# Optimization experiments

Measured on AMD Instinct MI355X. Metric: run time of the kernel, lower is better.

## Reference

```python
import jax, jax.numpy as jnp
import numpy as np

B_, L_, DIN, DM, DS, DR, K = 2, 1024, 1024, 2048, 16, 128, 4


def setup_inputs() -> dict:
    key = jax.random.key(0)
    ks = jax.random.split(key, 10)
    s = lambda k, shape, sc=0.02: (jax.random.normal(k, shape, jnp.float32) * sc)
    A_init = jnp.tile(jnp.arange(1, DS + 1, dtype=jnp.float32)[None, :], (DM, 1))  # (DM, DS)
    return {
        'x_in': jax.random.normal(ks[0], (B_, L_, DIN), jnp.float32),
        'W_in': s(ks[1], (DIN, DM)),
        'W_res': s(ks[2], (DIN, DM)),
        'W_out': s(ks[3], (DM, DIN)),
        'conv_w': s(ks[4], (DM, K), 0.1),   # depthwise conv weight (torch shape (DM,1,K) squeezed)
        'conv_b': jnp.zeros((DM,), jnp.float32),
        'A_log': jnp.log(A_init),
        'D': jnp.ones((DM,), jnp.float32),
        'W_B': s(ks[5], (DM, DS)),
        'W_C': s(ks[6], (DM, DS)),
        'W_dt': s(ks[7], (DM, DR)),
        'dt_w': s(ks[8], (DR, DM)),
        'dt_b': jnp.zeros((DM,), jnp.float32),
    }


def reference(x_in, W_in, W_res, W_out, conv_w, conv_b, A_log, D, W_B, W_C, W_dt, dt_w, dt_b):
    Bb, L, _ = x_in.shape
    x = x_in @ W_in                     # (B, L, DM)
    res = x_in @ W_res                  # (B, L, DM)
    # Causal depthwise conv1d: pad left k-1, truncate to L (matches Conv1d(padding=k-1)[:, :, :L])
    xp = jnp.pad(x, ((0, 0), (K - 1, 0), (0, 0)))
    xc = conv_b
    for i in range(K):
        xc = xc + xp[:, i:i + L, :] * conv_w[:, i]
    xc = jax.nn.silu(xc)                # (B, L, DM)
    # Selective SSM (fused_ssm)
    A = -jnp.exp(A_log)                 # (DM, DS)
    Bp = xc @ W_B                       # (B, L, DS)
    Cp = xc @ W_C                       # (B, L, DS)
    delta = jax.nn.softplus((xc @ W_dt) @ dt_w + dt_b)  # (B, L, DM)
    dA = jnp.exp(delta[..., None] * A)                       # (B, L, DM, DS)
    dBu = delta[..., None] * Bp[:, :, None, :] * xc[..., None]  # (B, L, DM, DS)

    def step(h, inp):
        dA_t, dBu_t, C_t = inp
        h = dA_t * h + dBu_t                         # (B, DM, DS)
        y = jnp.einsum('bdn,bn->bd', h, C_t)         # (B, DM)
        return h, y

    h0 = jnp.zeros((Bb, DM, DS), jnp.float32)
    _, ys = jax.lax.scan(step, h0, (dA.transpose(1, 0, 2, 3), dBu.transpose(1, 0, 2, 3), Cp.transpose(1, 0, 2)))
    y = ys.transpose(1, 0, 2) + D * xc  # (B, L, DM)
    y = y * jax.nn.silu(res)
    return y @ W_out                    # (B, L, DIN)
```

## Files before the change

### kernel.cpp

```cpp
#include <hip/hip_runtime.h>
#include <hip/hip_bf16.h>

constexpr int B_  = 2;
constexpr int L_  = 1024;
constexpr int DIN = 1024;
constexpr int DM  = 2048;
constexpr int DS  = 16;
constexpr int DR  = 128;
constexpr int KC  = 4;
constexpr int M_  = B_ * L_;
constexpr int NP2 = 256;
constexpr int NPC = 160;
constexpr int KSLICES = 8;
constexpr int KSL = DM / KSLICES;

constexpr int NC = 32;
constexpr int CL = L_ / NC;
constexpr int S_ = B_ * DM * DS;

typedef __bf16 bf16x8 __attribute__((ext_vector_type(8)));
typedef float  f32x4  __attribute__((ext_vector_type(4)));

__device__ __forceinline__ void gload_lds16(const void* g, void* l) {
    __builtin_amdgcn_global_load_lds(
        (const __attribute__((address_space(1))) void*)g,
        (__attribute__((address_space(3))) void*)l, 16, 0, 0);
}

__device__ __forceinline__ void transpose_block(const float* __restrict__ in,
                                                __bf16* __restrict__ out,
                                                int R, int C, int bx, int by, int t) {
    __shared__ float tile[32][33];
    int tx = t & 31, ty = t >> 5;
    #pragma unroll
    for (int j = 0; j < 32; j += 8)
        tile[ty + j][tx] = in[(size_t)(by * 32 + ty + j) * C + (bx * 32 + tx)];
    __syncthreads();
    #pragma unroll
    for (int j = 0; j < 32; j += 8)
        out[(size_t)(bx * 32 + ty + j) * R + (by * 32 + tx)] = (__bf16)tile[tx][ty + j];
}

__global__ void prep_all(const float* __restrict__ x_in, const float* __restrict__ W_in,
                         const float* __restrict__ W_res, const float* __restrict__ W_out,
                         const float* __restrict__ dt_w,
                         const float* __restrict__ W_B, const float* __restrict__ W_C,
                         const float* __restrict__ W_dt, const float* __restrict__ conv_w,
                         __bf16* __restrict__ xinB, __bf16* __restrict__ WinT,
                         __bf16* __restrict__ WresT, __bf16* __restrict__ WoutT,
                         __bf16* __restrict__ dtwT, __bf16* __restrict__ projW,
                         float* __restrict__ cwT) {
    int blk = blockIdx.x, t = threadIdx.x;
    if (blk < 8192) {
        int i = blk * 256 + t;
        xinB[i] = (__bf16)x_in[i];
    } else if (blk < 10240) {
        int b = blk - 8192;
        transpose_block(W_in, WinT, DIN, DM, b % 64, b / 64, t);
    } else if (blk < 12288) {
        int b = blk - 10240;
        transpose_block(W_res, WresT, DIN, DM, b % 64, b / 64, t);
    } else if (blk < 14336) {
        int b = blk - 12288;
        transpose_block(W_out, WoutT, DM, DIN, b % 32, b / 32, t);
    } else if (blk < 14592) {
        int b = blk - 14336;
        transpose_block(dt_w, dtwT, DR, DM, b % 64, b / 64, t);
    } else if (blk < 16640) {
        int i = (blk - 14592) * 256 + t;
        int k = i % DM;
        int n = i / DM;
        float v = 0.f;
        if (n < 16)        v = W_B[(size_t)k * DS + n];
        else if (n < 32)   v = W_C[(size_t)k * DS + (n - 16)];
        else if (n < 160)  v = W_dt[(size_t)k * DR + (n - 32)];
        projW[i] = (__bf16)v;
    } else {
        int j = (blk - 16640) * 256 + t;
        int tap = j / DM, d = j % DM;
        cwT[j] = conv_w[d * KC + tap];
    }
}

__global__ void reduce_split(const __bf16* __restrict__ PpartB, float* __restrict__ Bp,
                             float* __restrict__ Cp, __bf16* __restrict__ dtmpB) {
    int i = blockIdx.x * 256 + threadIdx.x;
    int row = i / NPC, c = i % NPC;
    float v = 0.f;
    #pragma unroll
    for (int ks = 0; ks < KSLICES; ks++)
        v += (float)PpartB[(size_t)ks * M_ * NPC + i];
    if (c < 16)       Bp[(size_t)row * DS + c] = v;
    else if (c < 32)  Cp[(size_t)row * DS + (c - 16)] = v;
    else              dtmpB[(size_t)row * DR + (c - 32)] = (__bf16)v;
}

template<int EPI>
__global__ void gemm_tile128(const __bf16* __restrict__ A, const __bf16* __restrict__ BT,
                             float* __restrict__ Cf, __bf16* __restrict__ Cb,
                             const float* __restrict__ bias, int M, int N, int K,
                             int lda, int ldb) {
    __shared__ __bf16 sA[2][2][128 * 32];
    __shared__ __bf16 sB[2][2][128 * 32];
    int t = threadIdx.x;
    int lane = t & 63, w = t >> 6;
    int wm = w >> 2, wn = w & 3;
    int m0 = blockIdx.y * 128, n0 = blockIdx.x * 128;
    int kbase = blockIdx.z * K;
    int q = lane >> 4, rr = lane & 15;

    f32x4 acc[4][2] = {};

    int srow = t >> 2;
    int slot = t & 3;

    const int nt = K >> 6;

    auto stage = [&](int kt, int bufi) {
        int gkb = slot ^ ((srow >> 1) & 3);
        #pragma unroll
        for (int s = 0; s < 2; s++) {
            gload_lds16(A  + (size_t)(m0 + srow) * lda + kbase + kt + s * 32 + gkb * 8,
                        &sA[bufi][s][w * 512]);
            gload_lds16(BT + (size_t)(n0 + srow) * ldb + kbase + kt + s * 32 + gkb * 8,
                        &sB[bufi][s][w * 512]);
        }
    };

    stage(0, 0);
    __syncthreads();

    int cur = 0;
    for (int tix = 0; tix < nt; tix++) {
        if (tix + 1 < nt) stage((tix + 1) << 6, cur ^ 1);

        #pragma unroll
        for (int s = 0; s < 2; s++) {
            bf16x8 af[4], bfr[2];
            #pragma unroll
            for (int i = 0; i < 4; i++) {
                int rowA = wm * 64 + i * 16 + rr;
                af[i] = *(const bf16x8*)(&sA[cur][s][rowA * 32 + ((q ^ ((rowA >> 1) & 3)) * 8)]);
            }
            #pragma unroll
            for (int j = 0; j < 2; j++) {
                int rowB = wn * 32 + j * 16 + rr;
                bfr[j] = *(const bf16x8*)(&sB[cur][s][rowB * 32 + ((q ^ ((rowB >> 1) & 3)) * 8)]);
            }
            #pragma unroll
            for (int i = 0; i < 4; i++)
                #pragma unroll
                for (int j = 0; j < 2; j++)
                    acc[i][j] = __builtin_amdgcn_mfma_f32_16x16x32_bf16(af[i], bfr[j], acc[i][j], 0, 0, 0);
        }

        __syncthreads();
        cur ^= 1;
    }

    #pragma unroll
    for (int i = 0; i < 4; i++) {
        #pragma unroll
        for (int j = 0; j < 2; j++) {
            int col = n0 + wn * 32 + j * 16 + rr;
            #pragma unroll
            for (int jj = 0; jj < 4; jj++) {
                int row = m0 + wm * 64 + i * 16 + q * 4 + jj;
                float v = acc[i][j][jj];
                if (EPI == 1) {
                    float z = v + bias[col];
                    Cb[(size_t)row * N + col] = (__bf16)((z > 20.f) ? z : log1pf(__expf(z)));
                } else if (EPI == 2) {
                    if (col < DM) ((__bf16*)Cf)[(size_t)row * DM + col] = (__bf16)v;
                    else          Cb[(size_t)row * DM + (col - DM)] = (__bf16)v;
                } else {
                    if (col < NPC)
                        Cb[(size_t)blockIdx.z * M * NPC + (size_t)row * NPC + col] = (__bf16)v;
                }
            }
        }
    }
}

__global__ void gemm_out64(const __bf16* __restrict__ A, const __bf16* __restrict__ BT,
                           float* __restrict__ C, int M, int N, int K, int lda, int ldb) {
    __shared__ __bf16 sA[2][2][128 * 32];
    __shared__ __bf16 sB[2][2][64 * 32];
    int t = threadIdx.x;
    int lane = t & 63, w = t >> 6;
    int wm = w >> 1, wn = w & 1;
    int m0 = blockIdx.y * 128, n0 = blockIdx.x * 64;
    int q = lane >> 4, rr = lane & 15;

    f32x4 acc[2][2] = {};
    int srow = t >> 2;
    int slot = t & 3;

    const int nt = K >> 6;

    auto stage = [&](int kt, int bufi) {
        int gkb = slot ^ ((srow >> 1) & 3);
        #pragma unroll
        for (int s = 0; s < 2; s++) {
            gload_lds16(A + (size_t)(m0 + srow) * lda + kt + s * 32 + gkb * 8,
                        &sA[bufi][s][w * 512]);
            if (t < 256)
                gload_lds16(BT + (size_t)(n0 + srow) * ldb + kt + s * 32 + gkb * 8,
                            &sB[bufi][s][w * 512]);
        }
    };

    stage(0, 0);
    __syncthreads();

    int cur = 0;
    for (int tix = 0; tix < nt; tix++) {
        if (tix + 1 < nt) stage((tix + 1) << 6, cur ^ 1);

        #pragma unroll
        for (int s = 0; s < 2; s++) {
            bf16x8 af[2], bfr[2];
            #pragma unroll
            for (int i = 0; i < 2; i++) {
                int rowA = wm * 32 + i * 16 + rr;
                af[i] = *(const bf16x8*)(&sA[cur][s][rowA * 32 + ((q ^ ((rowA >> 1) & 3)) * 8)]);
            }
            #pragma unroll
            for (int j = 0; j < 2; j++) {
                int rowB = wn * 32 + j * 16 + rr;
                bfr[j] = *(const bf16x8*)(&sB[cur][s][rowB * 32 + ((q ^ ((rowB >> 1) & 3)) * 8)]);
            }
            #pragma unroll
            for (int i = 0; i < 2; i++)
                #pragma unroll
                for (int j = 0; j < 2; j++)
                    acc[i][j] = __builtin_amdgcn_mfma_f32_16x16x32_bf16(af[i], bfr[j], acc[i][j], 0, 0, 0);
        }

        __syncthreads();
        cur ^= 1;
    }

    #pragma unroll
    for (int i = 0; i < 2; i++) {
        #pragma unroll
        for (int j = 0; j < 2; j++) {
            int col = n0 + wn * 32 + j * 16 + rr;
            #pragma unroll
            for (int jj = 0; jj < 4; jj++) {
                int row = m0 + wm * 32 + i * 16 + q * 4 + jj;
                C[(size_t)row * N + col] = acc[i][j][jj];
            }
        }
    }
}

__global__ void conv_silu(const __bf16* __restrict__ x, const float* __restrict__ cwT,
                          const float* __restrict__ bias, __bf16* __restrict__ xcB) {
    int row = blockIdx.x;
    int d   = threadIdx.x * 8;
    int l   = row % L_;
    size_t base = (size_t)row * DM + d;

    float acc[8];
    {
        const f32x4* b4 = (const f32x4*)(bias + d);
        f32x4 b0 = b4[0], b1 = b4[1];
        #pragma unroll
        for (int q = 0; q < 4; q++) { acc[q] = b0[q]; acc[4 + q] = b1[q]; }
    }
    #pragma unroll
    for (int i = 0; i < KC; i++) {
        int li = l - (KC - 1) + i;
        if (li >= 0) {
            bf16x8 xv = *(const bf16x8*)(x + base + (size_t)(i - (KC - 1)) * DM);
            const f32x4* w4 = (const f32x4*)(cwT + (size_t)i * DM + d);
            f32x4 w0 = w4[0], w1 = w4[1];
            #pragma unroll
            for (int q = 0; q < 4; q++) {
                acc[q]     = fmaf((float)xv[q],     w0[q], acc[q]);
                acc[4 + q] = fmaf((float)xv[4 + q], w1[q], acc[4 + q]);
            }
        }
    }
    bf16x8 out;
    #pragma unroll
    for (int q = 0; q < 8; q++) {
        float v = acc[q] / (1.f + __expf(-acc[q]));
        out[q] = (__bf16)v;
    }
    *(bf16x8*)(xcB + base) = out;
}

__global__ void scan_phase1(const __bf16* __restrict__ delta, const __bf16* __restrict__ xc,
                            const float* __restrict__ Bp, const float* __restrict__ A_log,
                            __bf16* __restrict__ aprodB, __bf16* __restrict__ cendB) {
    int blk = blockIdx.x;
    int c   = blk % NC;
    int rem = blk / NC;
    int dmt = rem % (DM / 256);
    int b   = rem / (DM / 256);
    int t   = threadIdx.x;
    int dm  = dmt * 256 + t;
    int l0  = c * CL;

    __shared__ float sB[CL * DS];
    sB[t]       = Bp[((size_t)b * L_ + l0) * DS + t];
    sB[t + 256] = Bp[((size_t)b * L_ + l0) * DS + t + 256];
    __syncthreads();

    float Aval[DS];
    {
        const f32x4* Ap = (const f32x4*)(A_log + (size_t)dm * DS);
        #pragma unroll
        for (int r4 = 0; r4 < 4; r4++) {
            f32x4 a = Ap[r4];
            #pragma unroll
            for (int q = 0; q < 4; q++) Aval[r4 * 4 + q] = -__expf(a[q]);
        }
    }

    float h[DS], ap[DS];
    #pragma unroll
    for (int i = 0; i < DS; i++) { h[i] = 0.f; ap[i] = 1.f; }

    size_t base = ((size_t)b * L_ + l0) * DM + dm;
    #pragma unroll 4
    for (int j = 0; j < CL; j++) {
        float dl  = (float)delta[base + (size_t)j * DM];
        float xv  = (float)xc[base + (size_t)j * DM];
        float cmn = dl * xv;
        const f32x4* sB4 = (const f32x4*)(sB + j * DS);
        #pragma unroll
        for (int r4 = 0; r4 < 4; r4++) {
            f32x4 bv = sB4[r4];
            #pragma unroll
            for (int q = 0; q < 4; q++) {
                int i = r4 * 4 + q;
                float dA = __expf(dl * Aval[i]);
                ap[i] *= dA;
                h[i] = fmaf(dA, h[i], cmn * bv[q]);
            }
        }
    }

    size_t s = ((size_t)(b * DM + dm)) * DS;
    #pragma unroll
    for (int r8 = 0; r8 < 2; r8++) {
        bf16x8 va, vh;
        #pragma unroll
        for (int q = 0; q < 8; q++) { va[q] = (__bf16)ap[r8 * 8 + q]; vh[q] = (__bf16)h[r8 * 8 + q]; }
        ((bf16x8*)(aprodB + (size_t)c * S_ + s))[r8] = va;
        ((bf16x8*)(cendB  + (size_t)c * S_ + s))[r8] = vh;
    }
}

__global__ void scan_phase2(const __bf16* __restrict__ aprodB, const __bf16* __restrict__ cendB,
                            __bf16* __restrict__ hinitB) {
    int u = blockIdx.x * 256 + threadIdx.x;
    float h = 0.f;
    #pragma unroll
    for (int c = 0; c < NC; c++) {
        float a  = (float)aprodB[(size_t)c * S_ + u];
        float ce = (float)cendB [(size_t)c * S_ + u];
        hinitB[(size_t)c * S_ + u] = (__bf16)h;
        h = fmaf(a, h, ce);
    }
}

__global__ void scan_phase3(const __bf16* __restrict__ delta, const __bf16* __restrict__ xc,
                            const float* __restrict__ Bp, const float* __restrict__ Cp,
                            const __bf16* __restrict__ res, const float* __restrict__ A_log,
                            const float* __restrict__ Dw, const __bf16* __restrict__ hinitB,
                            __bf16* __restrict__ ybar) {
    int blk = blockIdx.x;
    int c   = blk % NC;
    int rem = blk / NC;
    int dmt = rem % (DM / 256);
    int b   = rem / (DM / 256);
    int t   = threadIdx.x;
    int dm  = dmt * 256 + t;
    int l0  = c * CL;

    __shared__ float sB[CL * DS];
    __shared__ float sC[CL * DS];
    sB[t]       = Bp[((size_t)b * L_ + l0) * DS + t];
    sB[t + 256] = Bp[((size_t)b * L_ + l0) * DS + t + 256];
    sC[t]       = Cp[((size_t)b * L_ + l0) * DS + t];
    sC[t + 256] = Cp[((size_t)b * L_ + l0) * DS + t + 256];
    __syncthreads();

    float Aval[DS];
    {
        const f32x4* Ap = (const f32x4*)(A_log + (size_t)dm * DS);
        #pragma unroll
        for (int r4 = 0; r4 < 4; r4++) {
            f32x4 a = Ap[r4];
            #pragma unroll
            for (int q = 0; q < 4; q++) Aval[r4 * 4 + q] = -__expf(a[q]);
        }
    }
    float Dval = Dw[dm];

    float h[DS];
    {
        size_t s = ((size_t)(b * DM + dm)) * DS;
        #pragma unroll
        for (int r8 = 0; r8 < 2; r8++) {
            bf16x8 v = ((const bf16x8*)(hinitB + (size_t)c * S_ + s))[r8];
            #pragma unroll
            for (int q = 0; q < 8; q++) h[r8 * 8 + q] = (float)v[q];
        }
    }

    size_t base = ((size_t)b * L_ + l0) * DM + dm;
    #pragma unroll 4
    for (int j = 0; j < CL; j++) {
        float dl  = (float)delta[base + (size_t)j * DM];
        float xv  = (float)xc[base + (size_t)j * DM];
        float rv  = (float)res[base + (size_t)j * DM];
        float cmn = dl * xv;
        float y = 0.f;
        const f32x4* sB4 = (const f32x4*)(sB + j * DS);
        const f32x4* sC4 = (const f32x4*)(sC + j * DS);
        #pragma unroll
        for (int r4 = 0; r4 < 4; r4++) {
            f32x4 bv = sB4[r4];
            f32x4 cv = sC4[r4];
            #pragma unroll
            for (int q = 0; q < 4; q++) {
                int i = r4 * 4 + q;
                float dA = __expf(dl * Aval[i]);
                h[i] = fmaf(dA, h[i], cmn * bv[q]);
                y = fmaf(h[i], cv[q], y);
            }
        }
        float g = rv / (1.f + __expf(-rv));
        ybar[base + (size_t)j * DM] = (__bf16)((y + Dval * xv) * g);
    }
}

extern "C" void kernel_launch(void* const* d_in, const int* in_sizes, int n_in,
                              void* d_out, int out_size, void* d_ws, size_t ws_size,
                              hipStream_t stream) {
    const float* x_in   = (const float*)d_in[0];
    const float* W_in   = (const float*)d_in[1];
    const float* W_res  = (const float*)d_in[2];
    const float* W_out  = (const float*)d_in[3];
    const float* conv_w = (const float*)d_in[4];
    const float* conv_b = (const float*)d_in[5];
    const float* A_log  = (const float*)d_in[6];
    const float* Dw     = (const float*)d_in[7];
    const float* W_B    = (const float*)d_in[8];
    const float* W_C    = (const float*)d_in[9];
    const float* W_dt   = (const float*)d_in[10];
    const float* dt_w   = (const float*)d_in[11];
    const float* dt_b   = (const float*)d_in[12];

    float* ws_f = (float*)d_ws;
    float* Bp    = ws_f;
    float* Cp    = Bp + (size_t)M_ * DS;
    float* cwT   = Cp + (size_t)M_ * DS;
    __bf16* bf_base = (__bf16*)(cwT + (size_t)KC * DM);
    __bf16* ybar   = bf_base;
    __bf16* xinB   = ybar   + (size_t)M_ * DM;
    __bf16* WinT   = xinB   + (size_t)M_ * DIN;
    __bf16* WresT  = WinT   + (size_t)DM * DIN;
    __bf16* WoutT  = WresT  + (size_t)DM * DIN;
    __bf16* xB     = WoutT  + (size_t)DIN * DM;
    __bf16* xcB    = xB     + (size_t)M_ * DM;
    __bf16* projW  = xcB    + (size_t)M_ * DM;
    __bf16* dtwT   = projW  + (size_t)NP2 * DM;
    __bf16* dtmpB  = dtwT   + (size_t)DM * DR;
    __bf16* deltaB = dtmpB  + (size_t)M_ * DR;
    __bf16* resB   = deltaB + (size_t)M_ * DM;
    __bf16* aprodB = resB   + (size_t)M_ * DM;
    __bf16* cendB  = aprodB + (size_t)NC * S_;
    __bf16* hinitB = cendB  + (size_t)NC * S_;
    __bf16* PpartB = hinitB + (size_t)NC * S_;

    prep_all<<<16672, 256, 0, stream>>>(x_in, W_in, W_res, W_out, dt_w, W_B, W_C, W_dt,
                                        conv_w, xinB, WinT, WresT, WoutT, dtwT, projW, cwT);

    gemm_tile128<2><<<dim3((2 * DM) / 128, M_ / 128, 1), 512, 0, stream>>>(
        xinB, WinT, (float*)xB, resB, nullptr, M_, 2 * DM, DIN, DIN, DIN);

    conv_silu<<<M_, 256, 0, stream>>>(xB, cwT, conv_b, xcB);

    gemm_tile128<4><<<dim3(NP2 / 128, M_ / 128, KSLICES), 512, 0, stream>>>(
        xcB, projW, nullptr, PpartB, nullptr, M_, NP2, KSL, DM, DM);
    reduce_split<<<(M_ * NPC) / 256, 256, 0, stream>>>(PpartB, Bp, Cp, dtmpB);

    gemm_tile128<1><<<dim3(DM / 128, M_ / 128, 1), 512, 0, stream>>>(
        dtmpB, dtwT, nullptr, deltaB, dt_b, M_, DM, DR, DR, DR);

    int nblk = B_ * (DM / 256) * NC;
    scan_phase1<<<nblk, 256, 0, stream>>>(deltaB, xcB, Bp, A_log, aprodB, cendB);
    scan_phase2<<<S_ / 256, 256, 0, stream>>>(aprodB, cendB, hinitB);
    scan_phase3<<<nblk, 256, 0, stream>>>(deltaB, xcB, Bp, Cp, resB, A_log, Dw, hinitB, ybar);

    gemm_out64<<<dim3(DIN / 64, M_ / 128), 512, 0, stream>>>(
        ybar, WoutT, (float*)d_out, M_, DIN, DM, DM, DM);
}
```

Baseline: 246.6 us.

## Widen input GEMM tiles and split K across warps in output GEMM

Replaces the input projection GEMM with a dedicated kernel using 128x256 tiles, so each warp computes a 64x64 block and reuses more data per shared-memory load. The output GEMM now has each warp own a full 64x64 tile and handle a quarter of a 128-wide K chunk. The four partial sums are then reduced through shared memory in two steps. This trades more registers, more LDS use and extra synchronisation for fewer blocks on the input GEMM and higher MFMA density per loaded fragment.

```diff
diff --git a/kernel.cpp b/kernel.cpp
--- a/kernel.cpp
+++ b/kernel.cpp
@@ -95,6 +95,86 @@
     else              dtmpB[(size_t)row * DR + (c - 32)] = (__bf16)v;
 }
 
+__global__ void gemm_in(const __bf16* __restrict__ A, const __bf16* __restrict__ BT,
+                        __bf16* __restrict__ Cx, __bf16* __restrict__ Cres,
+                        int K, int lda, int ldb) {
+    __shared__ __bf16 sA[2][2][128 * 32];
+    __shared__ __bf16 sB[2][2][256 * 32];
+    int t = threadIdx.x;
+    int lane = t & 63, w = t >> 6;
+    int wm = w >> 2, wn = w & 3;
+    int m0 = blockIdx.y * 128, n0 = blockIdx.x * 256;
+    int q = lane >> 4, rr = lane & 15;
+
+    f32x4 acc[4][4] = {};
+    int srow = t >> 2;
+    int slot = t & 3;
+
+    const int nt = K >> 6;
+
+    auto stage = [&](int kt, int bufi) {
+        int gkbA = slot ^ ((srow >> 1) & 3);
+        #pragma unroll
+        for (int s = 0; s < 2; s++) {
+            gload_lds16(A + (size_t)(m0 + srow) * lda + kt + s * 32 + gkbA * 8,
+                        &sA[bufi][s][w * 512]);
+            #pragma unroll
+            for (int rnd = 0; rnd < 2; rnd++) {
+                int row = srow + rnd * 128;
+                int gkb = slot ^ ((row >> 1) & 3);
+                gload_lds16(BT + (size_t)(n0 + row) * ldb + kt + s * 32 + gkb * 8,
+                            &sB[bufi][s][rnd * 4096 + w * 512]);
+            }
+        }
+    };
+
+    stage(0, 0);
+    __syncthreads();
+
+    int cur = 0;
+    for (int tix = 0; tix < nt; tix++) {
+        if (tix + 1 < nt) stage((tix + 1) << 6, cur ^ 1);
+
+        #pragma unroll
+        for (int s = 0; s < 2; s++) {
+            bf16x8 af[4], bfr[4];
+            #pragma unroll
+            for (int i = 0; i < 4; i++) {
+                int rowA = wm * 64 + i * 16 + rr;
+                af[i] = *(const bf16x8*)(&sA[cur][s][rowA * 32 + ((q ^ ((rowA >> 1) & 3)) * 8)]);
+            }
+            #pragma unroll
+            for (int j = 0; j < 4; j++) {
+                int rowB = wn * 64 + j * 16 + rr;
+                bfr[j] = *(const bf16x8*)(&sB[cur][s][rowB * 32 + ((q ^ ((rowB >> 1) & 3)) * 8)]);
+            }
+            #pragma unroll
+            for (int i = 0; i < 4; i++)
+                #pragma unroll
+                for (int j = 0; j < 4; j++)
+                    acc[i][j] = __builtin_amdgcn_mfma_f32_16x16x32_bf16(af[i], bfr[j], acc[i][j], 0, 0, 0);
+        }
+
+        __syncthreads();
+        cur ^= 1;
+    }
+
+    #pragma unroll
+    for (int i = 0; i < 4; i++) {
+        #pragma unroll
+        for (int j = 0; j < 4; j++) {
+            int col = n0 + wn * 64 + j * 16 + rr;
+            #pragma unroll
+            for (int jj = 0; jj < 4; jj++) {
+                int row = m0 + wm * 64 + i * 16 + q * 4 + jj;
+                float v = acc[i][j][jj];
+                if (col < DM) Cx[(size_t)row * DM + col] = (__bf16)v;
+                else          Cres[(size_t)row * DM + (col - DM)] = (__bf16)v;
+            }
+        }
+    }
+}
+
 template<int EPI>
 __global__ void gemm_tile128(const __bf16* __restrict__ A, const __bf16* __restrict__ BT,
                              float* __restrict__ Cf, __bf16* __restrict__ Cb,
@@ -110,7 +190,6 @@
     int q = lane >> 4, rr = lane & 15;
 
     f32x4 acc[4][2] = {};
-
     int srow = t >> 2;
     int slot = t & 3;
 
@@ -170,9 +249,6 @@
                 if (EPI == 1) {
                     float z = v + bias[col];
                     Cb[(size_t)row * N + col] = (__bf16)((z > 20.f) ? z : log1pf(__expf(z)));
-                } else if (EPI == 2) {
-                    if (col < DM) ((__bf16*)Cf)[(size_t)row * DM + col] = (__bf16)v;
-                    else          Cb[(size_t)row * DM + (col - DM)] = (__bf16)v;
                 } else {
                     if (col < NPC)
                         Cb[(size_t)blockIdx.z * M * NPC + (size_t)row * NPC + col] = (__bf16)v;
@@ -184,24 +260,24 @@
 
 __global__ void gemm_out64(const __bf16* __restrict__ A, const __bf16* __restrict__ BT,
                            float* __restrict__ C, int M, int N, int K, int lda, int ldb) {
-    __shared__ __bf16 sA[2][2][128 * 32];
-    __shared__ __bf16 sB[2][2][64 * 32];
+    __shared__ __bf16 sA[2][4][128 * 32];
+    __shared__ __bf16 sB[2][4][64 * 32];
     int t = threadIdx.x;
     int lane = t & 63, w = t >> 6;
-    int wm = w >> 1, wn = w & 1;
+    int pos = w & 1, kg = w >> 1;
     int m0 = blockIdx.y * 128, n0 = blockIdx.x * 64;
     int q = lane >> 4, rr = lane & 15;
 
-    f32x4 acc[2][2] = {};
+    f32x4 acc[4][4] = {};
     int srow = t >> 2;
     int slot = t & 3;
 
-    const int nt = K >> 6;
+    const int nt = K >> 7;
 
     auto stage = [&](int kt, int bufi) {
         int gkb = slot ^ ((srow >> 1) & 3);
         #pragma unroll
-        for (int s = 0; s < 2; s++) {
+        for (int s = 0; s < 4; s++) {
             gload_lds16(A + (size_t)(m0 + srow) * lda + kt + s * 32 + gkb * 8,
                         &sA[bufi][s][w * 512]);
             if (t < 256)
@@ -215,41 +291,76 @@
 
     int cur = 0;
     for (int tix = 0; tix < nt; tix++) {
-        if (tix + 1 < nt) stage((tix + 1) << 6, cur ^ 1);
-
-        #pragma unroll
-        for (int s = 0; s < 2; s++) {
-            bf16x8 af[2], bfr[2];
-            #pragma unroll
-            for (int i = 0; i < 2; i++) {
-                int rowA = wm * 32 + i * 16 + rr;
-                af[i] = *(const bf16x8*)(&sA[cur][s][rowA * 32 + ((q ^ ((rowA >> 1) & 3)) * 8)]);
-            }
-            #pragma unroll
-            for (int j = 0; j < 2; j++) {
-                int rowB = wn * 32 + j * 16 + rr;
-                bfr[j] = *(const bf16x8*)(&sB[cur][s][rowB * 32 + ((q ^ ((rowB >> 1) & 3)) * 8)]);
-            }
-            #pragma unroll
-            for (int i = 0; i < 2; i++)
-                #pragma unroll
-                for (int j = 0; j < 2; j++)
-                    acc[i][j] = __builtin_amdgcn_mfma_f32_16x16x32_bf16(af[i], bfr[j], acc[i][j], 0, 0, 0);
-        }
+        if (tix + 1 < nt) stage((tix + 1) << 7, cur ^ 1);
+
+        bf16x8 af[4], bfr[4];
+        #pragma unroll
+        for (int i = 0; i < 4; i++) {
+            int rowA = pos * 64 + i * 16 + rr;
+            af[i] = *(const bf16x8*)(&sA[cur][kg][rowA * 32 + ((q ^ ((rowA >> 1) & 3)) * 8)]);
+        }
+        #pragma unroll
+        for (int j = 0; j < 4; j++) {
+            int rowB = j * 16 + rr;
+            bfr[j] = *(const bf16x8*)(&sB[cur][kg][rowB * 32 + ((q ^ ((rowB >> 1) & 3)) * 8)]);
+        }
+        #pragma unroll
+        for (int i = 0; i < 4; i++)
+            #pragma unroll
+            for (int j = 0; j < 4; j++)
+                acc[i][j] = __builtin_amdgcn_mfma_f32_16x16x32_bf16(af[i], bfr[j], acc[i][j], 0, 0, 0);
 
         __syncthreads();
         cur ^= 1;
     }
 
-    #pragma unroll
-    for (int i = 0; i < 2; i++) {
-        #pragma unroll
-        for (int j = 0; j < 2; j++) {
-            int col = n0 + wn * 32 + j * 16 + rr;
-            #pragma unroll
-            for (int jj = 0; jj < 4; jj++) {
-                int row = m0 + wm * 32 + i * 16 + q * 4 + jj;
-                C[(size_t)row * N + col] = acc[i][j][jj];
+    float* red = (float*)sA;
+    if (kg >= 2) {
+        int base = ((pos * 2 + (kg - 2)) * 64 + lane) * 64;
+        #pragma unroll
+        for (int i = 0; i < 4; i++)
+            #pragma unroll
+            for (int j = 0; j < 4; j++)
+                #pragma unroll
+                for (int jj = 0; jj < 4; jj++)
+                    red[base + (i * 4 + j) * 4 + jj] = acc[i][j][jj];
+    }
+    __syncthreads();
+    if (kg < 2) {
+        int base = ((pos * 2 + kg) * 64 + lane) * 64;
+        #pragma unroll
+        for (int i = 0; i < 4; i++)
+            #pragma unroll
+            for (int j = 0; j < 4; j++)
+                #pragma unroll
+                for (int jj = 0; jj < 4; jj++)
+                    acc[i][j][jj] += red[base + (i * 4 + j) * 4 + jj];
+    }
+    __syncthreads();
+    if (kg == 1) {
+        int base = ((pos * 2) * 64 + lane) * 64;
+        #pragma unroll
+        for (int i = 0; i < 4; i++)
+            #pragma unroll
+            for (int j = 0; j < 4; j++)
+                #pragma unroll
+                for (int jj = 0; jj < 4; jj++)
+                    red[base + (i * 4 + j) * 4 + jj] = acc[i][j][jj];
+    }
+    __syncthreads();
+    if (kg == 0) {
+        int base = ((pos * 2) * 64 + lane) * 64;
+        #pragma unroll
+        for (int i = 0; i < 4; i++) {
+            #pragma unroll
+            for (int j = 0; j < 4; j++) {
+                int col = n0 + j * 16 + rr;
+                #pragma unroll
+                for (int jj = 0; jj < 4; jj++) {
+                    float v = acc[i][j][jj] + red[base + (i * 4 + j) * 4 + jj];
+                    int row = m0 + pos * 64 + i * 16 + q * 4 + jj;
+                    C[(size_t)row * N + col] = v;
+                }
             }
         }
     }
@@ -482,8 +593,8 @@
     prep_all<<<16672, 256, 0, stream>>>(x_in, W_in, W_res, W_out, dt_w, W_B, W_C, W_dt,
                                         conv_w, xinB, WinT, WresT, WoutT, dtwT, projW, cwT);
 
-    gemm_tile128<2><<<dim3((2 * DM) / 128, M_ / 128, 1), 512, 0, stream>>>(
-        xinB, WinT, (float*)xB, resB, nullptr, M_, 2 * DM, DIN, DIN, DIN);
+    gemm_in<<<dim3((2 * DM) / 256, M_ / 128), 512, 0, stream>>>(
+        xinB, WinT, xB, resB, DIN, DIN, DIN);
 
     conv_silu<<<M_, 256, 0, stream>>>(xB, cwT, conv_b, xcB);
 
```

New measurement: 253.1 us. 2.6% more time.

## Use 1024-thread 128x128 GEMM tiles and split-K output GEMM with atomics

Applied to the files above, without the earlier changes.

The three 128x128-tile GEMMs now launch 1024 threads (16 waves). Each wave computes a 32x32 sub-tile instead of 32x64, and half the threads stage A while the other half stage B. The output projection GEMM is split into two K halves along grid z and accumulates into the output with float atomicAdd. The output buffer is zeroed inside the prep kernel so the atomics start from zero. This is meant to raise wave-level parallelism and fill more CUs on the small output GEMM, at the cost of atomic traffic, a nondeterministic summation order and possible register limits from the new launch bounds.

```diff
diff --git a/kernel.cpp b/kernel.cpp
--- a/kernel.cpp
+++ b/kernel.cpp
@@ -49,7 +49,7 @@
                          __bf16* __restrict__ xinB, __bf16* __restrict__ WinT,
                          __bf16* __restrict__ WresT, __bf16* __restrict__ WoutT,
                          __bf16* __restrict__ dtwT, __bf16* __restrict__ projW,
-                         float* __restrict__ cwT) {
+                         float* __restrict__ cwT, float* __restrict__ outz) {
     int blk = blockIdx.x, t = threadIdx.x;
     if (blk < 8192) {
         int i = blk * 256 + t;
@@ -75,10 +75,13 @@
         else if (n < 32)   v = W_C[(size_t)k * DS + (n - 16)];
         else if (n < 160)  v = W_dt[(size_t)k * DR + (n - 32)];
         projW[i] = (__bf16)v;
-    } else {
+    } else if (blk < 16672) {
         int j = (blk - 16640) * 256 + t;
         int tap = j / DM, d = j % DM;
         cwT[j] = conv_w[d * KC + tap];
+    } else {
+        int i = (blk - 16672) * 256 + t;
+        ((f32x4*)outz)[i] = f32x4{0.f, 0.f, 0.f, 0.f};
     }
 }
 
@@ -96,10 +99,11 @@
 }
 
 template<int EPI>
-__global__ void gemm_tile128(const __bf16* __restrict__ A, const __bf16* __restrict__ BT,
-                             float* __restrict__ Cf, __bf16* __restrict__ Cb,
-                             const float* __restrict__ bias, int M, int N, int K,
-                             int lda, int ldb) {
+__global__ __launch_bounds__(1024, 8)
+void gemm_tile128(const __bf16* __restrict__ A, const __bf16* __restrict__ BT,
+                  float* __restrict__ Cf, __bf16* __restrict__ Cb,
+                  const float* __restrict__ bias, int M, int N, int K,
+                  int lda, int ldb) {
     __shared__ __bf16 sA[2][2][128 * 32];
     __shared__ __bf16 sB[2][2][128 * 32];
     int t = threadIdx.x;
@@ -109,21 +113,26 @@
     int kbase = blockIdx.z * K;
     int q = lane >> 4, rr = lane & 15;
 
-    f32x4 acc[4][2] = {};
-
-    int srow = t >> 2;
-    int slot = t & 3;
+    f32x4 acc[2][2] = {};
 
     const int nt = K >> 6;
 
+    int t2 = t & 511;
+    int srow = t2 >> 2;
+    int slot = t2 & 3;
+    int gkb = slot ^ ((srow >> 1) & 3);
+
     auto stage = [&](int kt, int bufi) {
-        int gkb = slot ^ ((srow >> 1) & 3);
-        #pragma unroll
-        for (int s = 0; s < 2; s++) {
-            gload_lds16(A  + (size_t)(m0 + srow) * lda + kbase + kt + s * 32 + gkb * 8,
-                        &sA[bufi][s][w * 512]);
-            gload_lds16(BT + (size_t)(n0 + srow) * ldb + kbase + kt + s * 32 + gkb * 8,
-                        &sB[bufi][s][w * 512]);
+        if (t < 512) {
+            #pragma unroll
+            for (int s = 0; s < 2; s++)
+                gload_lds16(A + (size_t)(m0 + srow) * lda + kbase + kt + s * 32 + gkb * 8,
+                            &sA[bufi][s][w * 512]);
+        } else {
+            #pragma unroll
+            for (int s = 0; s < 2; s++)
+                gload_lds16(BT + (size_t)(n0 + srow) * ldb + kbase + kt + s * 32 + gkb * 8,
+                            &sB[bufi][s][(w - 8) * 512]);
         }
     };
 
@@ -136,10 +145,10 @@
 
         #pragma unroll
         for (int s = 0; s < 2; s++) {
-            bf16x8 af[4], bfr[2];
-            #pragma unroll
-            for (int i = 0; i < 4; i++) {
-                int rowA = wm * 64 + i * 16 + rr;
+            bf16x8 af[2], bfr[2];
+            #pragma unroll
+            for (int i = 0; i < 2; i++) {
+                int rowA = wm * 32 + i * 16 + rr;
                 af[i] = *(const bf16x8*)(&sA[cur][s][rowA * 32 + ((q ^ ((rowA >> 1) & 3)) * 8)]);
             }
             #pragma unroll
@@ -148,7 +157,7 @@
                 bfr[j] = *(const bf16x8*)(&sB[cur][s][rowB * 32 + ((q ^ ((rowB >> 1) & 3)) * 8)]);
             }
             #pragma unroll
-            for (int i = 0; i < 4; i++)
+            for (int i = 0; i < 2; i++)
                 #pragma unroll
                 for (int j = 0; j < 2; j++)
                     acc[i][j] = __builtin_amdgcn_mfma_f32_16x16x32_bf16(af[i], bfr[j], acc[i][j], 0, 0, 0);
@@ -159,13 +168,13 @@
     }
 
     #pragma unroll
-    for (int i = 0; i < 4; i++) {
+    for (int i = 0; i < 2; i++) {
         #pragma unroll
         for (int j = 0; j < 2; j++) {
             int col = n0 + wn * 32 + j * 16 + rr;
             #pragma unroll
             for (int jj = 0; jj < 4; jj++) {
-                int row = m0 + wm * 64 + i * 16 + q * 4 + jj;
+                int row = m0 + wm * 32 + i * 16 + q * 4 + jj;
                 float v = acc[i][j][jj];
                 if (EPI == 1) {
                     float z = v + bias[col];
@@ -190,22 +199,24 @@
     int lane = t & 63, w = t >> 6;
     int wm = w >> 1, wn = w & 1;
     int m0 = blockIdx.y * 128, n0 = blockIdx.x * 64;
+    int kh = K >> 1;
+    int kbase = blockIdx.z * kh;
     int q = lane >> 4, rr = lane & 15;
 
     f32x4 acc[2][2] = {};
     int srow = t >> 2;
     int slot = t & 3;
 
-    const int nt = K >> 6;
+    const int nt = kh >> 6;
 
     auto stage = [&](int kt, int bufi) {
         int gkb = slot ^ ((srow >> 1) & 3);
         #pragma unroll
         for (int s = 0; s < 2; s++) {
-            gload_lds16(A + (size_t)(m0 + srow) * lda + kt + s * 32 + gkb * 8,
+            gload_lds16(A + (size_t)(m0 + srow) * lda + kbase + kt + s * 32 + gkb * 8,
                         &sA[bufi][s][w * 512]);
             if (t < 256)
-                gload_lds16(BT + (size_t)(n0 + srow) * ldb + kt + s * 32 + gkb * 8,
+                gload_lds16(BT + (size_t)(n0 + srow) * ldb + kbase + kt + s * 32 + gkb * 8,
                             &sB[bufi][s][w * 512]);
         }
     };
@@ -249,7 +260,7 @@
             #pragma unroll
             for (int jj = 0; jj < 4; jj++) {
                 int row = m0 + wm * 32 + i * 16 + q * 4 + jj;
-                C[(size_t)row * N + col] = acc[i][j][jj];
+                atomicAdd(&C[(size_t)row * N + col], acc[i][j][jj]);
             }
         }
     }
@@ -479,19 +490,20 @@
     __bf16* hinitB = cendB  + (size_t)NC * S_;
     __bf16* PpartB = hinitB + (size_t)NC * S_;
 
-    prep_all<<<16672, 256, 0, stream>>>(x_in, W_in, W_res, W_out, dt_w, W_B, W_C, W_dt,
-                                        conv_w, xinB, WinT, WresT, WoutT, dtwT, projW, cwT);
-
-    gemm_tile128<2><<<dim3((2 * DM) / 128, M_ / 128, 1), 512, 0, stream>>>(
+    prep_all<<<18720, 256, 0, stream>>>(x_in, W_in, W_res, W_out, dt_w, W_B, W_C, W_dt,
+                                        conv_w, xinB, WinT, WresT, WoutT, dtwT, projW,
+                                        cwT, (float*)d_out);
+
+    gemm_tile128<2><<<dim3((2 * DM) / 128, M_ / 128, 1), 1024, 0, stream>>>(
         xinB, WinT, (float*)xB, resB, nullptr, M_, 2 * DM, DIN, DIN, DIN);
 
     conv_silu<<<M_, 256, 0, stream>>>(xB, cwT, conv_b, xcB);
 
-    gemm_tile128<4><<<dim3(NP2 / 128, M_ / 128, KSLICES), 512, 0, stream>>>(
+    gemm_tile128<4><<<dim3(NP2 / 128, M_ / 128, KSLICES), 1024, 0, stream>>>(
         xcB, projW, nullptr, PpartB, nullptr, M_, NP2, KSL, DM, DM);
     reduce_split<<<(M_ * NPC) / 256, 256, 0, stream>>>(PpartB, Bp, Cp, dtmpB);
 
-    gemm_tile128<1><<<dim3(DM / 128, M_ / 128, 1), 512, 0, stream>>>(
+    gemm_tile128<1><<<dim3(DM / 128, M_ / 128, 1), 1024, 0, stream>>>(
         dtmpB, dtwT, nullptr, deltaB, dt_b, M_, DM, DR, DR, DR);
 
     int nblk = B_ * (DM / 256) * NC;
@@ -499,6 +511,6 @@
     scan_phase2<<<S_ / 256, 256, 0, stream>>>(aprodB, cendB, hinitB);
     scan_phase3<<<nblk, 256, 0, stream>>>(deltaB, xcB, Bp, Cp, resB, A_log, Dw, hinitB, ybar);
 
-    gemm_out64<<<dim3(DIN / 64, M_ / 128), 512, 0, stream>>>(
+    gemm_out64<<<dim3(DIN / 64, M_ / 128, 2), 512, 0, stream>>>(
         ybar, WoutT, (float*)d_out, M_, DIN, DM, DM, DM);
 }
```

Measured after the change: 245.4 us. About the same (-0.5%).
